# Optimization experiments

Measured on AMD Instinct MI355X. Metric: run time of the kernel, lower is better.

Reference implementation:

```python
import jax, jax.numpy as jnp
import numpy as np

N, B, E, H, D, L, NT = 30000, 16, 60000, 128, 64, 2, 5


def _build_graph():
    rng = np.random.default_rng(0)
    ng = N // B
    row = rng.integers(0, N, size=E)
    g = row // ng
    col = g * ng + rng.integers(0, ng, size=E)  # bonds stay within a graph
    order = np.argsort(g, kind='stable')        # sort bonds by graph id
    row, col = row[order], col[order]
    edge_index = np.stack([row, col]).astype(np.int32)
    # bond graph: bonds adjacent iff they share an atom (vectorized _build_bond_graph)
    atoms = np.concatenate([row, col])
    bonds = np.concatenate([np.arange(E), np.arange(E)])
    o2 = np.argsort(atoms, kind='stable')
    sb = bonds[o2]
    counts = np.bincount(atoms, minlength=N)
    offs = np.concatenate([[0], np.cumsum(counts)[:-1]])
    sq = counts * counts
    total = int(sq.sum())
    gid = np.repeat(np.arange(N), sq)
    poff = np.concatenate([[0], np.cumsum(sq)[:-1]])
    pos = np.arange(total) - np.repeat(poff, sq)
    c, o = counts[gid], offs[gid]
    ii, jj = pos // c, pos % c
    mask = ii != jj
    bond_edge_index = np.stack([sb[o + ii][mask], sb[o + jj][mask]]).astype(np.int32)
    batch = np.repeat(np.arange(B), ng).astype(np.int32)
    return edge_index, bond_edge_index, batch


def setup_inputs() -> dict:
    edge_index, bond_edge_index, batch = _build_graph()
    key = jax.random.key(0)
    ks = jax.random.split(key, 16)
    s = 0.05
    n = lambda k, shp: jax.random.normal(k, shp, jnp.float32) * s
    return {
        'atom_features': jax.random.normal(ks[0], (N, H), jnp.float32),
        'atom_pos': jax.random.normal(ks[1], (N, 3), jnp.float32),
        'atomic_numbers': jax.random.randint(ks[2], (N,), 1, 20, jnp.int32),
        'batch': jnp.asarray(batch),
        'edge_index': jnp.asarray(edge_index),
        'bond_edge_index': jnp.asarray(bond_edge_index),
        'iw1': n(ks[3], (2 * H, D)), 'ib1': jnp.zeros((D,), jnp.float32),
        'iw2': n(ks[4], (D, D)), 'ib2': jnp.zeros((D,), jnp.float32),
        'emb': n(ks[5], (L, NT, D)),
        'mw1': n(ks[6], (L, 3 * D, D)), 'mb1': jnp.zeros((L, D), jnp.float32),
        'mw2': n(ks[7], (L, D, D)), 'mb2': jnp.zeros((L, D), jnp.float32),
        'uw1': n(ks[8], (L, 2 * D, D)), 'ub1': jnp.zeros((L, D), jnp.float32),
        'uw2': n(ks[9], (L, D, D)), 'ub2': jnp.zeros((L, D), jnp.float32),
        'num_graphs': B,
    }


def reference(atom_features, atom_pos, iw1, ib1, iw2, ib2, emb, mw1, mb1, mw2, mb2,
              uw1, ub1, uw2, ub2, atomic_numbers, batch, edge_index, bond_edge_index,
              num_graphs):
    row, col = edge_index
    hi, hj = atom_features[row], atom_features[col]  # [E, H] gathers
    # bond_init MLP
    x = jax.nn.silu(jnp.concatenate([hi, hj], -1) @ iw1 + ib1) @ iw2 + ib2  # [E, D]
    # _classify_bonds: cosine-similarity thresholds (order matters, matches torch)
    ni = jnp.maximum(jnp.linalg.norm(hi, axis=-1), 1e-8)
    nj = jnp.maximum(jnp.linalg.norm(hj, axis=-1), 1e-8)
    sim = jnp.sum(hi * hj, -1) / (ni * nj)
    bt = jnp.where(sim > 0.8, 1, 0)
    bt = jnp.where(sim > 0.9, 2, bt)
    bt = jnp.where(sim < 0.3, 3, bt)
    src, dst = bond_edge_index  # x_j = x[src], x_i = x[dst]; aggregate at dst
    nb = x.shape[0]
    deg = jax.ops.segment_sum(jnp.ones(src.shape, jnp.float32), dst, num_segments=nb)
    denom = jnp.maximum(deg, 1.0)[:, None]  # PyG mean aggr: 0 for isolated nodes
    for l in range(mw1.shape[0]):
        te = emb[l][bt]  # [E, D] bond-type embedding
        msg_in = jnp.concatenate([x[dst], x[src], te[dst]], -1)  # [BE, 3D]
        msg = jax.nn.silu(msg_in @ mw1[l] + mb1[l]) @ mw2[l] + mb2[l]
        aggr = jax.ops.segment_sum(msg, dst, num_segments=nb) / denom
        upd_in = jnp.concatenate([aggr, x], -1)
        x = x + jax.nn.silu(upd_in @ uw1[l] + ub1[l]) @ uw2[l] + ub2[l]
    # pooling: edges are sorted by graph, so repeat_interleave == batch[row]
    bond_batch = batch[row]
    cnt = jax.ops.segment_sum(jnp.ones((nb,), jnp.float32), bond_batch, num_segments=num_graphs)
    gfeat = jax.ops.segment_sum(x, bond_batch, num_segments=num_graphs) / jnp.maximum(cnt, 1.0)[:, None]
    return x, gfeat
```

## Files before the change

### kernel.cpp

```cpp
#include <hip/hip_runtime.h>
#include <cstdint>
#include <cstddef>

#define HDIM 128
#define DDIM 64
#define NTYPES 5
#define NGRAPHS 16
#define PCHUNK 128
#define EPB 64
#define APW 8

typedef __attribute__((ext_vector_type(8))) short short8;
typedef __attribute__((ext_vector_type(4))) float f32x4;

static __device__ __forceinline__ short8 as_s8(uint4 u) {
    return __builtin_bit_cast(short8, u);
}

static __device__ __forceinline__ float silu_f(float v) {
    return v * __builtin_amdgcn_rcpf(1.0f + __expf(-v));
}

static __device__ __forceinline__ float4 ld4(const float* p) {
    return *reinterpret_cast<const float4*>(p);
// ... 111 lines not shown
}

__global__ void __launch_bounds__(256) scatter_k(const int* __restrict__ bsrc,
                                                 const int* __restrict__ bdst,
                                                 int* __restrict__ cursor,
                                                 int* __restrict__ srclist, int BE) {
    int i = blockIdx.x * 256 + threadIdx.x;
    if (i < BE) {
        int d = bdst[i];
        int p = __hip_atomic_fetch_add(&cursor[d], 1, __ATOMIC_RELAXED,
                                       __HIP_MEMORY_SCOPE_AGENT);
        srclist[p] = bsrc[i];
    }
}

__global__ void __launch_bounds__(64) tt2_k(const float* __restrict__ emb,
                                            const float* __restrict__ mw1,
                                            const float* __restrict__ mb1,
                                            float* __restrict__ tt) {
    int b = blockIdx.x;
    int l = b / NTYPES, t = b % NTYPES, j = threadIdx.x;
    const float* embl = emb + (size_t)l * NTYPES * DDIM + (size_t)t * DDIM;
    const float* w1 = mw1 + (size_t)l * 192 * DDIM;
    float s = mb1[l * DDIM + j];
    #pragma unroll 8
    for (int k = 0; k < DDIM; ++k)
        s = fmaf(embl[k], w1[(HDIM + k) * DDIM + j], s);
    tt[(size_t)b * DDIM + j] = s;
}

__global__ void __launch_bounds__(64) fuse_k(const float* __restrict__ mw2,
                                             const float* __restrict__ mb2,
                                             const float* __restrict__ uw1,
                                             float* __restrict__ w2u,
                                             float* __restrict__ b2u) {
    int l = blockIdx.x >> 6, k = blockIdx.x & 63, j = threadIdx.x;
    const float* w2 = mw2 + (size_t)l * DDIM * DDIM;
    const float* u1 = uw1 + (size_t)l * 128 * DDIM;
    float s = 0.f;
    #pragma unroll 8
    for (int t = 0; t < DDIM; ++t)
        s = fmaf(w2[k * DDIM + t], u1[(size_t)t * DDIM + j], s);
    w2u[(size_t)l * DDIM * DDIM + (size_t)k * DDIM + j] = s;
    if (k == 0) {
        float b = 0.f;
        #pragma unroll 8
        for (int t = 0; t < DDIM; ++t)
            b = fmaf(mb2[l * DDIM + t], u1[(size_t)t * DDIM + j], b);
        b2u[l * DDIM + j] = b;
    }
}

__global__ void __launch_bounds__(64) packall_k(const float* __restrict__ w2u,
                                                const float* __restrict__ uw1,
                                                const float* __restrict__ uw2,
                                                const float* __restrict__ mw1,
                                                const float* __restrict__ iw2,
                                                uint4* __restrict__ fw2u,
                                                uint4* __restrict__ fu1b,
                                                uint4* __restrict__ fu2,
                                                uint4* __restrict__ fp,
                                                uint4* __restrict__ fiw2,
                                                uint4* __restrict__ fp0) {
    int b = blockIdx.x;
    int mat = b >> 3, jt = (b >> 1) & 3, ks = b & 1, l = threadIdx.x;
    const float* src;
    uint4* dst;
    switch (mat) {
        case 0: src = w2u;                         dst = fw2u;        break;
        case 1: src = w2u + 4096;                  dst = fw2u + 1024; break;
        case 2: src = uw1 + 64 * 64;               dst = fu1b;        break;
        case 3: src = uw1 + 128 * 64 + 64 * 64;    dst = fu1b + 1024; break;
        case 4: src = uw2;                         dst = fu2;         break;
        case 5: src = uw2 + 4096;                  dst = fu2 + 1024;  break;
        case 6: src = mw1 + (size_t)192 * 64;      dst = fp;          break;
        case 7: src = mw1 + (size_t)192 * 64 + 64 * 64; dst = fp + 1024; break;
        case 8: src = iw2;                         dst = fiw2;        break;
        case 9: src = mw1;                         dst = fp0;         break;
        default: src = mw1 + (size_t)64 * 64;      dst = fp0 + 1024;  break;
    }
    int k0 = ks * 32 + (l >> 4) * 8;
    int j = jt * 16 + (l & 15);
    float f[8];
    #pragma unroll
    for (int i = 0; i < 8; ++i) f[i] = src[(size_t)(k0 + i) * 64 + j];
    uint4 h, lo;
    hilo8(f, h, lo);
    size_t di = ((size_t)(jt * 2 + ks) * 64 + l) * 2;
    dst[di] = h;
    dst[di + 1] = lo;
}

static __device__ __forceinline__ int slotIdx(int row, int slot) {
    return row * 8 + (slot ^ (row & 7));
}

static __device__ __forceinline__ short8 ldFragA(const uint4* buf, int rowBase, int lane, int ks) {
    int row = rowBase + (lane & 15);
    int slot = ks * 4 + (lane >> 4);
    return as_s8(buf[slotIdx(row, slot)]);
// ... 60 lines not shown
            nrm[a] = fmaf(hv.z, hv.z, nrm[a]);
            nrm[a] = fmaf(hv.w, hv.w, nrm[a]);
        }
    }
    #pragma unroll
    for (int a = 0; a < APW; ++a) {
        int atom = abase + a;
        if (atom < N) {
            pa[(size_t)atom * DDIM + lane] = accp[a];
            qa[(size_t)atom * DDIM + lane] = accq[a];
            if (lane == 0) na[atom] = sqrtf(nrm[a]);
        }
    }
}

__global__ void __launch_bounds__(512, 4) bond_init2_k(
    const float* __restrict__ AF, const int* __restrict__ row, const int* __restrict__ col,
    const float* __restrict__ pa, const float* __restrict__ qa, const float* __restrict__ na,
    const float* __restrict__ b1, const uint4* __restrict__ fW2, const float* __restrict__ b2,
    const uint4* __restrict__ fP0,
    float* __restrict__ x, int* __restrict__ bt,
    float* __restrict__ pd, uint4* __restrict__ ps, int E) {
    __shared__ uint4 sAhi[512];
    __shared__ uint4 sAlo[512];
    __shared__ uint4 sXhi[512];
    __shared__ uint4 sXlo[512];
    int nEB = (E + EPB - 1) / EPB;
    int lb = xcd_logical_block();
    if (lb >= nEB) return;
    int tid = threadIdx.x;
    int lane = tid & 63;
    int w = __builtin_amdgcn_readfirstlane((int)(tid >> 6));
    int e0 = lb * EPB;

    {
        int dl = tid >> 3, q = tid & 7;
        int d = e0 + dl;
        bool ok = d < E;
        int dd = ok ? d : 0;
        int r = row[dd], c = col[dd];
        int jq = q * 8;

        const float* hi = AF + (size_t)r * HDIM + q * 16;
        const float* hj = AF + (size_t)c * HDIM + q * 16;
        float dt = 0.f;
        #pragma unroll
        for (int k = 0; k < 16; k += 4) {
            float4 a4 = ld4(hi + k), b4 = ld4(hj + k);
            dt += a4.x * b4.x + a4.y * b4.y + a4.z * b4.z + a4.w * b4.w;
        }
        dt += __shfl_xor(dt, 1, 64);
        dt += __shfl_xor(dt, 2, 64);
        dt += __shfl_xor(dt, 4, 64);
        if (q == 0 && ok) {
            float nr = fmaxf(na[r], 1e-8f), nc = fmaxf(na[c], 1e-8f);
            float sim = dt / (nr * nc);
            int t = 0;
            if (sim > 0.8f) t = 1;
            if (sim > 0.9f) t = 2;
            if (sim < 0.3f) t = 3;
            bt[d] = t;
        }

        const float* pr = pa + (size_t)r * DDIM + jq;
        const float* qc = qa + (size_t)c * DDIM + jq;
        float4 p0 = ld4(pr + 0), p1 = ld4(pr + 4);
        float4 q0 = ld4(qc + 0), q1 = ld4(qc + 4);
        float hv[8];
        hv[0] = silu_f(p0.x + q0.x + b1[jq + 0]);
        hv[1] = silu_f(p0.y + q0.y + b1[jq + 1]);
        hv[2] = silu_f(p0.z + q0.z + b1[jq + 2]);
        hv[3] = silu_f(p0.w + q0.w + b1[jq + 3]);
        hv[4] = silu_f(p1.x + q1.x + b1[jq + 4]);
        hv[5] = silu_f(p1.y + q1.y + b1[jq + 5]);
        hv[6] = silu_f(p1.z + q1.z + b1[jq + 6]);
        hv[7] = silu_f(p1.w + q1.w + b1[jq + 7]);
        if (!ok) {
            #pragma unroll
            for (int i = 0; i < 8; ++i) hv[i] = 0.f;
        }
        uint4 h4, l4;
        hilo8(hv, h4, l4);
        int si = slotIdx(dl, q);
        sAhi[si] = h4; sAlo[si] = l4;
    }
    int jt = w & 3, mh = w >> 2;
    short8 W2h0, W2h1, W2l0, W2l1;
    loadB(fW2, jt, lane, W2h0, W2h1, W2l0, W2l1);
    __syncthreads();

    int rb0 = mh * 32, rb1 = mh * 32 + 16;
    f32x4 z4 = {0.f, 0.f, 0.f, 0.f};
    f32x4 acc0 = z4, acc1 = z4;
    acc0 = gemm_tile(sAhi, sAlo, rb0, lane, W2h0, W2h1, W2l0, W2l1, acc0);
    acc1 = gemm_tile(sAhi, sAlo, rb1, lane, W2h0, W2h1, W2l0, W2l1, acc1);
    int j = jt * 16 + (lane & 15);
    float b2j = b2[j];
    unsigned short* hX = (unsigned short*)sXhi;
    unsigned short* lX = (unsigned short*)sXlo;
    #pragma unroll
    for (int r = 0; r < 4; ++r) {
        int rowi = rb0 + (lane >> 4) * 4 + r;
        int e = e0 + rowi;
        float xn = acc0[r] + b2j;
        if (e < E) x[(size_t)e * DDIM + j] = xn;
        unsigned int hb = bf16r(xn);
        float lov = xn - __uint_as_float(hb << 16);
        int ui = (rowi * 8 + ((j >> 3) ^ (rowi & 7))) * 8 + (j & 7);
        hX[ui] = (unsigned short)hb;
        lX[ui] = (unsigned short)bf16r(lov);
    }
    #pragma unroll
    for (int r = 0; r < 4; ++r) {
        int rowi = rb1 + (lane >> 4) * 4 + r;
        int e = e0 + rowi;
        float xn = acc1[r] + b2j;
        if (e < E) x[(size_t)e * DDIM + j] = xn;
        unsigned int hb = bf16r(xn);
        float lov = xn - __uint_as_float(hb << 16);
        int ui = (rowi * 8 + ((j >> 3) ^ (rowi & 7))) * 8 + (j & 7);
        hX[ui] = (unsigned short)hb;
        lX[ui] = (unsigned short)bf16r(lov);
    }
    __syncthreads();

    const uint4* fPw = (w < 4) ? fP0 : (fP0 + 1024);
    int jp = w & 3;
    short8 Ph0, Ph1, Pl0, Pl1;
    loadB(fPw, jp, lane, Ph0, Ph1, Pl0, Pl1);
    f32x4 q0 = z4, q1 = z4, q2 = z4, q3 = z4;
    q0 = gemm_tile(sXhi, sXlo, 0,  lane, Ph0, Ph1, Pl0, Pl1, q0);
    q1 = gemm_tile(sXhi, sXlo, 16, lane, Ph0, Ph1, Pl0, Pl1, q1);
    q2 = gemm_tile(sXhi, sXlo, 32, lane, Ph0, Ph1, Pl0, Pl1, q2);
    q3 = gemm_tile(sXhi, sXlo, 48, lane, Ph0, Ph1, Pl0, Pl1, q3);
    unsigned short* hA = (unsigned short*)sAhi;
    if (w < 4) {
        int jd = jp * 16 + (lane & 15);
        #pragma unroll
        for (int mt = 0; mt < 4; ++mt) {
            f32x4 qq = (mt == 0) ? q0 : (mt == 1) ? q1 : (mt == 2) ? q2 : q3;
            #pragma unroll
            for (int r = 0; r < 4; ++r) {
                int rowi = mt * 16 + (lane >> 4) * 4 + r;
                int e = e0 + rowi;
                if (e < E) pd[(size_t)e * DDIM + jd] = qq[r];
            }
        }
    } else {
        int js = jp * 16 + (lane & 15);
        #pragma unroll
        for (int mt = 0; mt < 4; ++mt) {
            f32x4 qq = (mt == 0) ? q0 : (mt == 1) ? q1 : (mt == 2) ? q2 : q3;
            #pragma unroll
            for (int r = 0; r < 4; ++r) {
                int rowi = mt * 16 + (lane >> 4) * 4 + r;
                int ui = (rowi * 8 + ((js >> 3) ^ (rowi & 7))) * 8 + (js & 7);
                hA[ui] = (unsigned short)bf16r(qq[r]);
            }
        }
    }
    __syncthreads();
    {
        int dl = tid >> 3, q = tid & 7;
        int d = e0 + dl;
        if (d < E) ps[(size_t)d * 8 + q] = sAhi[slotIdx(dl, q)];
    }
}

__global__ void __launch_bounds__(256) proj_k(const float* __restrict__ x,
                                              const float* __restrict__ w1 ,
                                              float* __restrict__ pd, uint4* __restrict__ ps,
                                              int E) {
    int lane = threadIdx.x & 63;
    int w = __builtin_amdgcn_readfirstlane((int)(threadIdx.x >> 6));
    int e = blockIdx.x * EPB + lane;
    bool ok = e < E;
    int eidx = ok ? e : 0;
// ... 18 lines not shown
                aps[jj] = fmaf(xv[kk], wsv[jj], aps[jj]);
            }
        }
    }
    if (ok) {
        float* pr = pd + (size_t)e * DDIM + j0;
        st4(pr + 0,  make_float4(apd[0],  apd[1],  apd[2],  apd[3]));
        st4(pr + 4,  make_float4(apd[4],  apd[5],  apd[6],  apd[7]));
        st4(pr + 8,  make_float4(apd[8],  apd[9],  apd[10], apd[11]));
        st4(pr + 12, make_float4(apd[12], apd[13], apd[14], apd[15]));
        ps[(size_t)e * 8 + 2 * w + 0] = pack8(aps + 0);
        ps[(size_t)e * 8 + 2 * w + 1] = pack8(aps + 8);
    }
}

__global__ void __launch_bounds__(512, 4) layer_k(
    float* __restrict__ x, const float* __restrict__ pd, const uint4* __restrict__ ps,
    const float* __restrict__ tt_l, const int* __restrict__ bt,
    const int* __restrict__ offs, const int* __restrict__ srclist,
    const int* __restrict__ cnt,
    const uint4* __restrict__ fW2u, const float* __restrict__ b2u,
    const uint4* __restrict__ fU1b, const float* __restrict__ ub1,
    const uint4* __restrict__ fU2, const float* __restrict__ ub2,
    const uint4* __restrict__ fP ,
    float* __restrict__ pdn, uint4* __restrict__ psn, int E) {
    __shared__ uint4 sAhi[512];
    __shared__ uint4 sAlo[512];
    __shared__ uint4 sXhi[512];
    __shared__ uint4 sXlo[512];
    __shared__ float degLDS[64];
    int nEB = (E + EPB - 1) / EPB;
    int lb = xcd_logical_block();
    if (lb >= nEB) return;
    int tid = threadIdx.x;
    int lane = tid & 63;
    int w = __builtin_amdgcn_readfirstlane((int)(tid >> 6));
    int e0 = lb * EPB;

    {
        int dl = tid >> 3, q = tid & 7;
        int d = e0 + dl;
        bool ok = d < E;
        int dd = ok ? d : 0;
        int jq = q * 8;
        const float* xr = x + (size_t)dd * DDIM + jq;
        float4 xv0 = ld4(xr + 0), xv1 = ld4(xr + 4);
        int dc = cnt[dd];
        const float* pr = pd + (size_t)dd * DDIM + jq;
        const float* tp = tt_l + (size_t)bt[dd] * DDIM + jq;
        float4 b0 = add4(ld4(pr + 0), ld4(tp + 0));
        float4 b1 = add4(ld4(pr + 4), ld4(tp + 4));
        float4 s0 = make_float4(0, 0, 0, 0), s1 = s0;
        int p0 = ok ? offs[d] : 0, p1 = ok ? offs[d + 1] : 0;
        int p = p0;
        for (; p + 4 <= p1; p += 4) {
            uint4 u0 = ps[(size_t)srclist[p + 0] * 8 + q];
            uint4 u1 = ps[(size_t)srclist[p + 1] * 8 + q];
            uint4 u2 = ps[(size_t)srclist[p + 2] * 8 + q];
            uint4 u3 = ps[(size_t)srclist[p + 3] * 8 + q];
            float4 a, b;
            unpack8(u0, a, b);
            silu_acc4(s0, add4(b0, a));
            silu_acc4(s1, add4(b1, b));
            unpack8(u1, a, b);
            silu_acc4(s0, add4(b0, a));
            silu_acc4(s1, add4(b1, b));
            unpack8(u2, a, b);
            silu_acc4(s0, add4(b0, a));
            silu_acc4(s1, add4(b1, b));
            unpack8(u3, a, b);
            silu_acc4(s0, add4(b0, a));
            silu_acc4(s1, add4(b1, b));
        }
        for (; p < p1; ++p) {
            uint4 u0 = ps[(size_t)srclist[p] * 8 + q];
            float4 a, b;
            unpack8(u0, a, b);
            silu_acc4(s0, add4(b0, a));
            silu_acc4(s1, add4(b1, b));
        }
        float inv = 1.0f / fmaxf((float)dc, 1.0f);
        float sv[8] = {s0.x * inv, s0.y * inv, s0.z * inv, s0.w * inv,
                       s1.x * inv, s1.y * inv, s1.z * inv, s1.w * inv};
        float xf[8] = {xv0.x, xv0.y, xv0.z, xv0.w, xv1.x, xv1.y, xv1.z, xv1.w};
        if (!ok) {
            #pragma unroll
            for (int i = 0; i < 8; ++i) { sv[i] = 0.f; xf[i] = 0.f; }
        }
        uint4 h4, l4;
        int si = slotIdx(dl, q);
        hilo8(sv, h4, l4);
        sAhi[si] = h4; sAlo[si] = l4;
        hilo8(xf, h4, l4);
        sXhi[si] = h4; sXlo[si] = l4;
        if (q == 0) degLDS[dl] = (ok && dc > 0) ? 1.0f : 0.0f;
    }
    int jt = w & 3, mh = w >> 2;
    short8 A2h0, A2h1, A2l0, A2l1;
    short8 U1h0, U1h1, U1l0, U1l1;
    loadB(fW2u, jt, lane, A2h0, A2h1, A2l0, A2l1);
    loadB(fU1b, jt, lane, U1h0, U1h1, U1l0, U1l1);
    __syncthreads();

    int rb0 = mh * 32, rb1 = mh * 32 + 16;
    f32x4 z4 = {0.f, 0.f, 0.f, 0.f};
    f32x4 acc0 = z4, acc1 = z4;
    acc0 = gemm_tile(sAhi, sAlo, rb0, lane, A2h0, A2h1, A2l0, A2l1, acc0);
    acc0 = gemm_tile(sXhi, sXlo, rb0, lane, U1h0, U1h1, U1l0, U1l1, acc0);
    acc1 = gemm_tile(sAhi, sAlo, rb1, lane, A2h0, A2h1, A2l0, A2l1, acc1);
    acc1 = gemm_tile(sXhi, sXlo, rb1, lane, U1h0, U1h1, U1l0, U1l1, acc1);
    __syncthreads();
    int j = jt * 16 + (lane & 15);
    float ub1j = ub1[j], b2uj = b2u[j];
    unsigned short* hA = (unsigned short*)sAhi;
    unsigned short* lA = (unsigned short*)sAlo;
    #pragma unroll
    for (int r = 0; r < 4; ++r) {
        int row = rb0 + (lane >> 4) * 4 + r;
        float hv = silu_f(acc0[r] + ub1j + degLDS[row] * b2uj);
        unsigned int hb = bf16r(hv);
        float lov = hv - __uint_as_float(hb << 16);
        int ui = (row * 8 + ((j >> 3) ^ (row & 7))) * 8 + (j & 7);
        hA[ui] = (unsigned short)hb;
        lA[ui] = (unsigned short)bf16r(lov);
    }
    #pragma unroll
    for (int r = 0; r < 4; ++r) {
        int row = rb1 + (lane >> 4) * 4 + r;
        float hv = silu_f(acc1[r] + ub1j + degLDS[row] * b2uj);
        unsigned int hb = bf16r(hv);
        float lov = hv - __uint_as_float(hb << 16);
        int ui = (row * 8 + ((j >> 3) ^ (row & 7))) * 8 + (j & 7);
        hA[ui] = (unsigned short)hb;
        lA[ui] = (unsigned short)bf16r(lov);
    }
    __syncthreads();

    short8 U2h0, U2h1, U2l0, U2l1;
    loadB(fU2, jt, lane, U2h0, U2h1, U2l0, U2l1);
    f32x4 o0 = z4, o1 = z4;
    o0 = gemm_tile(sAhi, sAlo, rb0, lane, U2h0, U2h1, U2l0, U2l1, o0);
    o1 = gemm_tile(sAhi, sAlo, rb1, lane, U2h0, U2h1, U2l0, U2l1, o1);
    float ub2j = ub2[j];
    bool haveP = (fP != nullptr);
    unsigned short* hX = (unsigned short*)sXhi;
    unsigned short* lX = (unsigned short*)sXlo;
    #pragma unroll
    for (int r = 0; r < 4; ++r) {
        int row = rb0 + (lane >> 4) * 4 + r;
        int e = e0 + row;
        float xvv = (e < E) ? x[(size_t)e * DDIM + j] : 0.f;
        float xn = xvv + o0[r] + ub2j;
        if (e < E) x[(size_t)e * DDIM + j] = xn;
        if (haveP) {
            unsigned int hb = bf16r(xn);
            float lov = xn - __uint_as_float(hb << 16);
            int ui = (row * 8 + ((j >> 3) ^ (row & 7))) * 8 + (j & 7);
            hX[ui] = (unsigned short)hb;
            lX[ui] = (unsigned short)bf16r(lov);
        }
    }
    #pragma unroll
    for (int r = 0; r < 4; ++r) {
        int row = rb1 + (lane >> 4) * 4 + r;
        int e = e0 + row;
        float xvv = (e < E) ? x[(size_t)e * DDIM + j] : 0.f;
        float xn = xvv + o1[r] + ub2j;
        if (e < E) x[(size_t)e * DDIM + j] = xn;
        if (haveP) {
            unsigned int hb = bf16r(xn);
            float lov = xn - __uint_as_float(hb << 16);
            int ui = (row * 8 + ((j >> 3) ^ (row & 7))) * 8 + (j & 7);
            hX[ui] = (unsigned short)hb;
            lX[ui] = (unsigned short)bf16r(lov);
        }
    }
    if (!haveP) return;
    __syncthreads();

    const uint4* fPw = (w < 4) ? fP : (fP + 1024);
    int jp = w & 3;
    short8 Ph0, Ph1, Pl0, Pl1;
    loadB(fPw, jp, lane, Ph0, Ph1, Pl0, Pl1);
    f32x4 q0 = z4, q1 = z4, q2 = z4, q3 = z4;
    q0 = gemm_tile(sXhi, sXlo, 0,  lane, Ph0, Ph1, Pl0, Pl1, q0);
    q1 = gemm_tile(sXhi, sXlo, 16, lane, Ph0, Ph1, Pl0, Pl1, q1);
    q2 = gemm_tile(sXhi, sXlo, 32, lane, Ph0, Ph1, Pl0, Pl1, q2);
    q3 = gemm_tile(sXhi, sXlo, 48, lane, Ph0, Ph1, Pl0, Pl1, q3);
    if (w < 4) {
        int jd = jp * 16 + (lane & 15);
        #pragma unroll
        for (int mt = 0; mt < 4; ++mt) {
            f32x4 qq = (mt == 0) ? q0 : (mt == 1) ? q1 : (mt == 2) ? q2 : q3;
            #pragma unroll
            for (int r = 0; r < 4; ++r) {
                int row = mt * 16 + (lane >> 4) * 4 + r;
                int e = e0 + row;
                if (e < E) pdn[(size_t)e * DDIM + jd] = qq[r];
            }
        }
    } else {
        int js = jp * 16 + (lane & 15);
        #pragma unroll
        for (int mt = 0; mt < 4; ++mt) {
            f32x4 qq = (mt == 0) ? q0 : (mt == 1) ? q1 : (mt == 2) ? q2 : q3;
            #pragma unroll
            for (int r = 0; r < 4; ++r) {
                int row = mt * 16 + (lane >> 4) * 4 + r;
                int ui = (row * 8 + ((js >> 3) ^ (row & 7))) * 8 + (js & 7);
                hA[ui] = (unsigned short)bf16r(qq[r]);
            }
        }
    }
    __syncthreads();
    {
        int dl = tid >> 3, q = tid & 7;
        int d = e0 + dl;
        if (d < E) psn[(size_t)d * 8 + q] = sAhi[slotIdx(dl, q)];
    }
}

__global__ void __launch_bounds__(256) pool_k(
    const float* __restrict__ x, const int* __restrict__ row,
    const int* __restrict__ batch, float* __restrict__ gfeat, int E) {
    int lane = threadIdx.x & 63;
    int esub = threadIdx.x >> 6;
    int e0 = blockIdx.x * PCHUNK;
    int e1 = min(e0 + PCHUNK, E);
    float sum = 0.f;
    int cur = -1;
// ... 58 lines not shown

    const int N  = in_sizes[0] / HDIM;
    const int E  = in_sizes[4] / 2;
    const int BE = in_sizes[5] / 2;
    const int NB = (E + 255) / 256;
    const int EB = (E + EPB - 1) / EPB;
    const int AB = (N + 4 * APW - 1) / (4 * APW);
    const int EBS = ((EB + 7) / 8) * 8;
    const int PB = (E + PCHUNK - 1) / PCHUNK;

    float* xout  = (float*)d_out;
    float* gfeat = xout + (size_t)E * DDIM;

    char* w = (char*)d_ws;
    float* tt       = (float*)w;  w += sizeof(float) * 2 * NTYPES * DDIM;
    float* w2u      = (float*)w;  w += sizeof(float) * 2 * DDIM * DDIM;
    float* b2u      = (float*)w;  w += sizeof(float) * 2 * DDIM;
    w = (char*)(((uintptr_t)w + 15) & ~(uintptr_t)15);
    uint4* fW2u     = (uint4*)w;  w += 2048 * sizeof(uint4);
    uint4* fU1b     = (uint4*)w;  w += 2048 * sizeof(uint4);
    uint4* fU2      = (uint4*)w;  w += 2048 * sizeof(uint4);
    uint4* fP       = (uint4*)w;  w += 2048 * sizeof(uint4);
    uint4* fIw2     = (uint4*)w;  w += 1024 * sizeof(uint4);
    uint4* fP0      = (uint4*)w;  w += 2048 * sizeof(uint4);
    int*   cnt      = (int*)w;    w += sizeof(int) * E;
    int*   offs     = (int*)w;    w += sizeof(int) * (E + 1);
    int*   cursor   = (int*)w;    w += sizeof(int) * E;
    int*   bt       = (int*)w;    w += sizeof(int) * E;
    int*   bsum     = (int*)w;    w += sizeof(int) * 1024;
    int*   bpre     = (int*)w;    w += sizeof(int) * 1024;
    int*   srclist  = (int*)w;    w += sizeof(int) * BE;
// ... 8 lines not shown
    uint4* ps2      = (uint4*)w;  w += sizeof(unsigned short) * (size_t)E * DDIM;
    bool fuse_proj = ((size_t)(w - (char*)d_ws) <= ws_size);

    const int* row  = edge_index;
    const int* col  = edge_index + E;
    const int* bsrc = bond_edge_index;
    const int* bdst = bond_edge_index + BE;

    hipMemsetAsync(cnt, 0, (size_t)E * sizeof(int), stream);
    count_k<<<(BE + 255) / 256, 256, 0, stream>>>(bdst, cnt, BE);
    bsum_k<<<NB, 256, 0, stream>>>(cnt, bsum, E);
    bscan_k<<<1, 1024, 0, stream>>>(bsum, bpre, NB);
    offs_k<<<NB, 256, 0, stream>>>(cnt, bpre, offs, cursor, E);
    scatter_k<<<(BE + 255) / 256, 256, 0, stream>>>(bsrc, bdst, cursor, srclist, BE);

    tt2_k<<<2 * NTYPES, 64, 0, stream>>>(emb, mw1, mb1, tt);
    fuse_k<<<2 * 64, 64, 0, stream>>>(mw2, mb2, uw1, w2u, b2u);
    packall_k<<<88, 64, 0, stream>>>(w2u, uw1, uw2, mw1, iw2,
                                     fW2u, fU1b, fU2, fP, fIw2, fP0);

    atom_proj_k<<<AB, 256, 0, stream>>>(AF, iw1, pa, qa, na, N);
    bond_init2_k<<<EBS, 512, 0, stream>>>(AF, row, col, pa, qa, na, ib1, fIw2, ib2,
                                          fP0, xout, bt, pd, ps, E);

    if (fuse_proj) {
        layer_k<<<EBS, 512, 0, stream>>>(
            xout, pd, ps, tt, bt, offs, srclist, cnt,
            fW2u, b2u, fU1b, ub1, fU2, ub2,
            fP, pd2, ps2, E);
        layer_k<<<EBS, 512, 0, stream>>>(
            xout, pd2, ps2, tt + NTYPES * DDIM, bt, offs, srclist, cnt,
            fW2u + 1024, b2u + DDIM, fU1b + 1024, ub1 + DDIM,
            fU2 + 1024, ub2 + DDIM,
            nullptr, nullptr, nullptr, E);
    } else {
        for (int l = 0; l < 2; ++l) {
            if (l > 0)
                proj_k<<<EB, 256, 0, stream>>>(xout, mw1 + (size_t)l * 192 * 64, pd, ps, E);
            layer_k<<<EBS, 512, 0, stream>>>(
                xout, pd, ps, tt + (size_t)l * NTYPES * DDIM, bt, offs, srclist, cnt,
                fW2u + (size_t)l * 1024, b2u + (size_t)l * DDIM,
                fU1b + (size_t)l * 1024, ub1 + (size_t)l * DDIM,
                fU2 + (size_t)l * 1024, ub2 + (size_t)l * DDIM,
                nullptr, nullptr, nullptr, E);
        }
    }

    hipMemsetAsync(gfeat, 0, NGRAPHS * DDIM * sizeof(float), stream);
    pool_k<<<PB, 256, 0, stream>>>(xout, row, batch, gfeat, E);
    pool_final_k<<<NGRAPHS, 64, 0, stream>>>(row, batch, gfeat, E);
}
```

Baseline: 319.6 us.

## Double threads per block in bond and layer kernels; merge weight prep kernels

The bond-init and layer kernels move from 512 to 1024 threads per block. Each bond row now uses two threads: they split the neighbor gather loop, the dot product and the projection loads, and combine results with lane shuffles. Each wave in the MFMA stages now handles one 16-row tile instead of two. The three weight-prep kernels merge into a single prep kernel that also computes the fused W2·U1 product inline. The aim is more memory-level parallelism in the irregular gather and fewer launches, at the cost of extra shuffles and higher register pressure under the tighter launch bounds.

```diff
diff --git a/kernel.cpp b/kernel.cpp
--- a/kernel.cpp
+++ b/kernel.cpp
@@ -149,76 +149,79 @@
     }
 }
 
-__global__ void __launch_bounds__(64) tt2_k(const float* __restrict__ emb,
-                                            const float* __restrict__ mw1,
-                                            const float* __restrict__ mb1,
-                                            float* __restrict__ tt) {
-    int b = blockIdx.x;
-    int l = b / NTYPES, t = b % NTYPES, j = threadIdx.x;
-    const float* embl = emb + (size_t)l * NTYPES * DDIM + (size_t)t * DDIM;
-    const float* w1 = mw1 + (size_t)l * 192 * DDIM;
-    float s = mb1[l * DDIM + j];
-    #pragma unroll 8
-    for (int k = 0; k < DDIM; ++k)
-        s = fmaf(embl[k], w1[(HDIM + k) * DDIM + j], s);
-    tt[(size_t)b * DDIM + j] = s;
-}
-
-__global__ void __launch_bounds__(64) fuse_k(const float* __restrict__ mw2,
+__global__ void __launch_bounds__(64) prep_k(const float* __restrict__ emb,
+                                             const float* __restrict__ mw1,
+                                             const float* __restrict__ mb1,
+                                             const float* __restrict__ mw2,
                                              const float* __restrict__ mb2,
                                              const float* __restrict__ uw1,
-                                             float* __restrict__ w2u,
-                                             float* __restrict__ b2u) {
-    int l = blockIdx.x >> 6, k = blockIdx.x & 63, j = threadIdx.x;
-    const float* w2 = mw2 + (size_t)l * DDIM * DDIM;
-    const float* u1 = uw1 + (size_t)l * 128 * DDIM;
-    float s = 0.f;
-    #pragma unroll 8
-    for (int t = 0; t < DDIM; ++t)
-        s = fmaf(w2[k * DDIM + t], u1[(size_t)t * DDIM + j], s);
-    w2u[(size_t)l * DDIM * DDIM + (size_t)k * DDIM + j] = s;
-    if (k == 0) {
-        float b = 0.f;
+                                             const float* __restrict__ uw2,
+                                             const float* __restrict__ iw2,
+                                             float* __restrict__ tt,
+                                             float* __restrict__ b2u,
+                                             uint4* __restrict__ fw2u,
+                                             uint4* __restrict__ fu1b,
+                                             uint4* __restrict__ fu2,
+                                             uint4* __restrict__ fp,
+                                             uint4* __restrict__ fiw2,
+                                             uint4* __restrict__ fp0) {
+    int b = blockIdx.x;
+    int l = threadIdx.x;
+    if (b < 10) {
+        int ll = b / NTYPES, t = b % NTYPES;
+        const float* embl = emb + (size_t)ll * NTYPES * DDIM + (size_t)t * DDIM;
+        const float* w1 = mw1 + (size_t)ll * 192 * DDIM;
+        float s = mb1[ll * DDIM + l];
+        #pragma unroll 8
+        for (int k = 0; k < DDIM; ++k)
+            s = fmaf(embl[k], w1[(HDIM + k) * DDIM + l], s);
+        tt[(size_t)b * DDIM + l] = s;
+        return;
+    }
+    if (b < 12) {
+        int ll = b - 10;
+        const float* u1 = uw1 + (size_t)ll * 128 * DDIM;
+        float s = 0.f;
         #pragma unroll 8
         for (int t = 0; t < DDIM; ++t)
-            b = fmaf(mb2[l * DDIM + t], u1[(size_t)t * DDIM + j], b);
-        b2u[l * DDIM + j] = b;
-    }
-}
-
-__global__ void __launch_bounds__(64) packall_k(const float* __restrict__ w2u,
-                                                const float* __restrict__ uw1,
-                                                const float* __restrict__ uw2,
-                                                const float* __restrict__ mw1,
-                                                const float* __restrict__ iw2,
-                                                uint4* __restrict__ fw2u,
-                                                uint4* __restrict__ fu1b,
-                                                uint4* __restrict__ fu2,
-                                                uint4* __restrict__ fp,
-                                                uint4* __restrict__ fiw2,
-                                                uint4* __restrict__ fp0) {
-    int b = blockIdx.x;
-    int mat = b >> 3, jt = (b >> 1) & 3, ks = b & 1, l = threadIdx.x;
-    const float* src;
-    uint4* dst;
-    switch (mat) {
-        case 0: src = w2u;                         dst = fw2u;        break;
-        case 1: src = w2u + 4096;                  dst = fw2u + 1024; break;
-        case 2: src = uw1 + 64 * 64;               dst = fu1b;        break;
-        case 3: src = uw1 + 128 * 64 + 64 * 64;    dst = fu1b + 1024; break;
-        case 4: src = uw2;                         dst = fu2;         break;
-        case 5: src = uw2 + 4096;                  dst = fu2 + 1024;  break;
-        case 6: src = mw1 + (size_t)192 * 64;      dst = fp;          break;
-        case 7: src = mw1 + (size_t)192 * 64 + 64 * 64; dst = fp + 1024; break;
-        case 8: src = iw2;                         dst = fiw2;        break;
-        case 9: src = mw1;                         dst = fp0;         break;
-        default: src = mw1 + (size_t)64 * 64;      dst = fp0 + 1024;  break;
-    }
+            s = fmaf(mb2[ll * DDIM + t], u1[(size_t)t * DDIM + l], s);
+        b2u[ll * DDIM + l] = s;
+        return;
+    }
+    int pb = b - 12;
+    int mat = pb >> 3, jt = (pb >> 1) & 3, ks = pb & 1;
     int k0 = ks * 32 + (l >> 4) * 8;
     int j = jt * 16 + (l & 15);
     float f[8];
-    #pragma unroll
-    for (int i = 0; i < 8; ++i) f[i] = src[(size_t)(k0 + i) * 64 + j];
+    uint4* dst;
+    if (mat <= 1) {
+        const float* w2 = mw2 + (size_t)mat * DDIM * DDIM;
+        const float* u1 = uw1 + (size_t)mat * 128 * DDIM;
+        #pragma unroll
+        for (int i = 0; i < 8; ++i) {
+            float s = 0.f;
+            #pragma unroll 8
+            for (int t = 0; t < DDIM; ++t)
+                s = fmaf(w2[(size_t)(k0 + i) * DDIM + t], u1[(size_t)t * DDIM + j], s);
+            f[i] = s;
+        }
+        dst = fw2u + (size_t)mat * 1024;
+    } else {
+        const float* src;
+        switch (mat) {
+            case 2:  src = uw1 + 64 * 64;                   dst = fu1b;        break;
+            case 3:  src = uw1 + 128 * 64 + 64 * 64;        dst = fu1b + 1024; break;
+            case 4:  src = uw2;                             dst = fu2;         break;
+            case 5:  src = uw2 + 4096;                      dst = fu2 + 1024;  break;
+            case 6:  src = mw1 + (size_t)192 * 64;          dst = fp;          break;
+            case 7:  src = mw1 + (size_t)192 * 64 + 64 * 64; dst = fp + 1024;  break;
+            case 8:  src = iw2;                             dst = fiw2;        break;
+            case 9:  src = mw1;                             dst = fp0;         break;
+            default: src = mw1 + (size_t)64 * 64;           dst = fp0 + 1024;  break;
+        }
+        #pragma unroll
+        for (int i = 0; i < 8; ++i) f[i] = src[(size_t)(k0 + i) * DDIM + j];
+    }
     uint4 h, lo;
     hilo8(f, h, lo);
     size_t di = ((size_t)(jt * 2 + ks) * 64 + l) * 2;
@@ -309,7 +312,7 @@
     }
 }
 
-__global__ void __launch_bounds__(512, 4) bond_init2_k(
+__global__ void __launch_bounds__(1024, 8) bond_init2_k(
     const float* __restrict__ AF, const int* __restrict__ row, const int* __restrict__ col,
     const float* __restrict__ pa, const float* __restrict__ qa, const float* __restrict__ na,
     const float* __restrict__ b1, const uint4* __restrict__ fW2, const float* __restrict__ b2,
@@ -329,25 +332,24 @@
     int e0 = lb * EPB;
 
     {
-        int dl = tid >> 3, q = tid & 7;
+        int dl = tid >> 4, q = (tid >> 1) & 7, h = tid & 1;
         int d = e0 + dl;
         bool ok = d < E;
         int dd = ok ? d : 0;
         int r = row[dd], c = col[dd];
         int jq = q * 8;
 
-        const float* hi = AF + (size_t)r * HDIM + q * 16;
-        const float* hj = AF + (size_t)c * HDIM + q * 16;
-        float dt = 0.f;
-        #pragma unroll
-        for (int k = 0; k < 16; k += 4) {
-            float4 a4 = ld4(hi + k), b4 = ld4(hj + k);
-            dt += a4.x * b4.x + a4.y * b4.y + a4.z * b4.z + a4.w * b4.w;
-        }
+        const float* hi = AF + (size_t)r * HDIM + q * 16 + h * 8;
+        const float* hj = AF + (size_t)c * HDIM + q * 16 + h * 8;
+        float4 a4 = ld4(hi), a5 = ld4(hi + 4);
+        float4 b4 = ld4(hj), b5 = ld4(hj + 4);
+        float dt = a4.x * b4.x + a4.y * b4.y + a4.z * b4.z + a4.w * b4.w
+                 + a5.x * b5.x + a5.y * b5.y + a5.z * b5.z + a5.w * b5.w;
         dt += __shfl_xor(dt, 1, 64);
         dt += __shfl_xor(dt, 2, 64);
         dt += __shfl_xor(dt, 4, 64);
-        if (q == 0 && ok) {
+        dt += __shfl_xor(dt, 8, 64);
+        if (q == 0 && h == 0 && ok) {
             float nr = fmaxf(na[r], 1e-8f), nc = fmaxf(na[c], 1e-8f);
             float sim = dt / (nr * nc);
             int t = 0;
@@ -357,47 +359,53 @@
             bt[d] = t;
         }
 
-        const float* pr = pa + (size_t)r * DDIM + jq;
-        const float* qc = qa + (size_t)c * DDIM + jq;
-        float4 p0 = ld4(pr + 0), p1 = ld4(pr + 4);
-        float4 q0 = ld4(qc + 0), q1 = ld4(qc + 4);
-        float hv[8];
-        hv[0] = silu_f(p0.x + q0.x + b1[jq + 0]);
-        hv[1] = silu_f(p0.y + q0.y + b1[jq + 1]);
-        hv[2] = silu_f(p0.z + q0.z + b1[jq + 2]);
-        hv[3] = silu_f(p0.w + q0.w + b1[jq + 3]);
-        hv[4] = silu_f(p1.x + q1.x + b1[jq + 4]);
-        hv[5] = silu_f(p1.y + q1.y + b1[jq + 5]);
-        hv[6] = silu_f(p1.z + q1.z + b1[jq + 6]);
-        hv[7] = silu_f(p1.w + q1.w + b1[jq + 7]);
-        if (!ok) {
-            #pragma unroll
-            for (int i = 0; i < 8; ++i) hv[i] = 0.f;
-        }
-        uint4 h4, l4;
-        hilo8(hv, h4, l4);
-        int si = slotIdx(dl, q);
-        sAhi[si] = h4; sAlo[si] = l4;
-    }
-    int jt = w & 3, mh = w >> 2;
+        const float* srcv = h ? (qa + (size_t)c * DDIM + jq) : (pa + (size_t)r * DDIM + jq);
+        float4 v0 = ld4(srcv), v1 = ld4(srcv + 4);
+        v0.x += __shfl_xor(v0.x, 1, 64);
+        v0.y += __shfl_xor(v0.y, 1, 64);
+        v0.z += __shfl_xor(v0.z, 1, 64);
+        v0.w += __shfl_xor(v0.w, 1, 64);
+        v1.x += __shfl_xor(v1.x, 1, 64);
+        v1.y += __shfl_xor(v1.y, 1, 64);
+        v1.z += __shfl_xor(v1.z, 1, 64);
+        v1.w += __shfl_xor(v1.w, 1, 64);
+        if (h == 0) {
+            float hv[8];
+            hv[0] = silu_f(v0.x + b1[jq + 0]);
+            hv[1] = silu_f(v0.y + b1[jq + 1]);
+            hv[2] = silu_f(v0.z + b1[jq + 2]);
+            hv[3] = silu_f(v0.w + b1[jq + 3]);
+            hv[4] = silu_f(v1.x + b1[jq + 4]);
+            hv[5] = silu_f(v1.y + b1[jq + 5]);
+            hv[6] = silu_f(v1.z + b1[jq + 6]);
+            hv[7] = silu_f(v1.w + b1[jq + 7]);
+            if (!ok) {
+                #pragma unroll
+                for (int i = 0; i < 8; ++i) hv[i] = 0.f;
+            }
+            uint4 h4, l4;
+            hilo8(hv, h4, l4);
+            int si = slotIdx(dl, q);
+            sAhi[si] = h4; sAlo[si] = l4;
+        }
+    }
+    int jt = w & 3, rt = (w >> 2) & 3;
     short8 W2h0, W2h1, W2l0, W2l1;
     loadB(fW2, jt, lane, W2h0, W2h1, W2l0, W2l1);
     __syncthreads();
 
-    int rb0 = mh * 32, rb1 = mh * 32 + 16;
+    int rb = rt * 16;
     f32x4 z4 = {0.f, 0.f, 0.f, 0.f};
-    f32x4 acc0 = z4, acc1 = z4;
-    acc0 = gemm_tile(sAhi, sAlo, rb0, lane, W2h0, W2h1, W2l0, W2l1, acc0);
-    acc1 = gemm_tile(sAhi, sAlo, rb1, lane, W2h0, W2h1, W2l0, W2l1, acc1);
+    f32x4 acc = gemm_tile(sAhi, sAlo, rb, lane, W2h0, W2h1, W2l0, W2l1, z4);
     int j = jt * 16 + (lane & 15);
     float b2j = b2[j];
     unsigned short* hX = (unsigned short*)sXhi;
     unsigned short* lX = (unsigned short*)sXlo;
     #pragma unroll
     for (int r = 0; r < 4; ++r) {
-        int rowi = rb0 + (lane >> 4) * 4 + r;
+        int rowi = rb + (lane >> 4) * 4 + r;
         int e = e0 + rowi;
-        float xn = acc0[r] + b2j;
+        float xn = acc[r] + b2j;
         if (e < E) x[(size_t)e * DDIM + j] = xn;
         unsigned int hb = bf16r(xn);
         float lov = xn - __uint_as_float(hb << 16);
@@ -405,38 +413,24 @@
         hX[ui] = (unsigned short)hb;
         lX[ui] = (unsigned short)bf16r(lov);
     }
-    #pragma unroll
-    for (int r = 0; r < 4; ++r) {
-        int rowi = rb1 + (lane >> 4) * 4 + r;
-        int e = e0 + rowi;
-        float xn = acc1[r] + b2j;
-        if (e < E) x[(size_t)e * DDIM + j] = xn;
-        unsigned int hb = bf16r(xn);
-        float lov = xn - __uint_as_float(hb << 16);
-        int ui = (rowi * 8 + ((j >> 3) ^ (rowi & 7))) * 8 + (j & 7);
-        hX[ui] = (unsigned short)hb;
-        lX[ui] = (unsigned short)bf16r(lov);
-    }
-    __syncthreads();
-
-    const uint4* fPw = (w < 4) ? fP0 : (fP0 + 1024);
+    __syncthreads();
+
+    int c8 = w & 7, rt2 = w >> 3;
+    const uint4* fPw = (c8 < 4) ? fP0 : (fP0 + 1024);
     int jp = w & 3;
     short8 Ph0, Ph1, Pl0, Pl1;
     loadB(fPw, jp, lane, Ph0, Ph1, Pl0, Pl1);
-    f32x4 q0 = z4, q1 = z4, q2 = z4, q3 = z4;
-    q0 = gemm_tile(sXhi, sXlo, 0,  lane, Ph0, Ph1, Pl0, Pl1, q0);
-    q1 = gemm_tile(sXhi, sXlo, 16, lane, Ph0, Ph1, Pl0, Pl1, q1);
-    q2 = gemm_tile(sXhi, sXlo, 32, lane, Ph0, Ph1, Pl0, Pl1, q2);
-    q3 = gemm_tile(sXhi, sXlo, 48, lane, Ph0, Ph1, Pl0, Pl1, q3);
+    f32x4 q0 = gemm_tile(sXhi, sXlo, rt2 * 32, lane, Ph0, Ph1, Pl0, Pl1, z4);
+    f32x4 q1 = gemm_tile(sXhi, sXlo, rt2 * 32 + 16, lane, Ph0, Ph1, Pl0, Pl1, z4);
     unsigned short* hA = (unsigned short*)sAhi;
-    if (w < 4) {
+    if (c8 < 4) {
         int jd = jp * 16 + (lane & 15);
         #pragma unroll
-        for (int mt = 0; mt < 4; ++mt) {
-            f32x4 qq = (mt == 0) ? q0 : (mt == 1) ? q1 : (mt == 2) ? q2 : q3;
+        for (int mt = 0; mt < 2; ++mt) {
+            f32x4 qq = (mt == 0) ? q0 : q1;
             #pragma unroll
             for (int r = 0; r < 4; ++r) {
-                int rowi = mt * 16 + (lane >> 4) * 4 + r;
+                int rowi = rt2 * 32 + mt * 16 + (lane >> 4) * 4 + r;
                 int e = e0 + rowi;
                 if (e < E) pd[(size_t)e * DDIM + jd] = qq[r];
             }
@@ -444,18 +438,18 @@
     } else {
         int js = jp * 16 + (lane & 15);
         #pragma unroll
-        for (int mt = 0; mt < 4; ++mt) {
-            f32x4 qq = (mt == 0) ? q0 : (mt == 1) ? q1 : (mt == 2) ? q2 : q3;
+        for (int mt = 0; mt < 2; ++mt) {
+            f32x4 qq = (mt == 0) ? q0 : q1;
             #pragma unroll
             for (int r = 0; r < 4; ++r) {
-                int rowi = mt * 16 + (lane >> 4) * 4 + r;
+                int rowi = rt2 * 32 + mt * 16 + (lane >> 4) * 4 + r;
                 int ui = (rowi * 8 + ((js >> 3) ^ (rowi & 7))) * 8 + (js & 7);
                 hA[ui] = (unsigned short)bf16r(qq[r]);
             }
         }
     }
     __syncthreads();
-    {
+    if (tid < 512) {
         int dl = tid >> 3, q = tid & 7;
         int d = e0 + dl;
         if (d < E) ps[(size_t)d * 8 + q] = sAhi[slotIdx(dl, q)];
@@ -504,7 +498,7 @@
     }
 }
 
-__global__ void __launch_bounds__(512, 4) layer_k(
+__global__ void __launch_bounds__(1024, 8) layer_k(
     float* __restrict__ x, const float* __restrict__ pd, const uint4* __restrict__ ps,
     const float* __restrict__ tt_l, const int* __restrict__ bt,
     const int* __restrict__ offs, const int* __restrict__ srclist,
@@ -528,77 +522,85 @@
     int e0 = lb * EPB;
 
     {
-        int dl = tid >> 3, q = tid & 7;
+        int dl = tid >> 4, q = (tid >> 1) & 7, h = tid & 1;
         int d = e0 + dl;
         bool ok = d < E;
         int dd = ok ? d : 0;
         int jq = q * 8;
-        const float* xr = x + (size_t)dd * DDIM + jq;
-        float4 xv0 = ld4(xr + 0), xv1 = ld4(xr + 4);
+        float4 xv0 = {0.f, 0.f, 0.f, 0.f}, xv1 = xv0;
+        if (h) {
+            const float* xr = x + (size_t)dd * DDIM + jq;
+            xv0 = ld4(xr + 0); xv1 = ld4(xr + 4);
+        }
         int dc = cnt[dd];
         const float* pr = pd + (size_t)dd * DDIM + jq;
         const float* tp = tt_l + (size_t)bt[dd] * DDIM + jq;
         float4 b0 = add4(ld4(pr + 0), ld4(tp + 0));
-        float4 b1 = add4(ld4(pr + 4), ld4(tp + 4));
+        float4 bb1 = add4(ld4(pr + 4), ld4(tp + 4));
         float4 s0 = make_float4(0, 0, 0, 0), s1 = s0;
         int p0 = ok ? offs[d] : 0, p1 = ok ? offs[d + 1] : 0;
-        int p = p0;
-        for (; p + 4 <= p1; p += 4) {
+        int p = p0 + h;
+        for (; p + 2 < p1; p += 4) {
             uint4 u0 = ps[(size_t)srclist[p + 0] * 8 + q];
-            uint4 u1 = ps[(size_t)srclist[p + 1] * 8 + q];
-            uint4 u2 = ps[(size_t)srclist[p + 2] * 8 + q];
-            uint4 u3 = ps[(size_t)srclist[p + 3] * 8 + q];
+            uint4 u1 = ps[(size_t)srclist[p + 2] * 8 + q];
             float4 a, b;
             unpack8(u0, a, b);
             silu_acc4(s0, add4(b0, a));
-            silu_acc4(s1, add4(b1, b));
+            silu_acc4(s1, add4(bb1, b));
             unpack8(u1, a, b);
             silu_acc4(s0, add4(b0, a));
-            silu_acc4(s1, add4(b1, b));
-            unpack8(u2, a, b);
-            silu_acc4(s0, add4(b0, a));
-            silu_acc4(s1, add4(b1, b));
-            unpack8(u3, a, b);
-            silu_acc4(s0, add4(b0, a));
-            silu_acc4(s1, add4(b1, b));
-        }
-        for (; p < p1; ++p) {
+            silu_acc4(s1, add4(bb1, b));
+        }
+        for (; p < p1; p += 2) {
             uint4 u0 = ps[(size_t)srclist[p] * 8 + q];
             float4 a, b;
             unpack8(u0, a, b);
             silu_acc4(s0, add4(b0, a));
-            silu_acc4(s1, add4(b1, b));
-        }
+            silu_acc4(s1, add4(bb1, b));
+        }
+        s0.x += __shfl_xor(s0.x, 1, 64);
+        s0.y += __shfl_xor(s0.y, 1, 64);
+        s0.z += __shfl_xor(s0.z, 1, 64);
+        s0.w += __shfl_xor(s0.w, 1, 64);
+        s1.x += __shfl_xor(s1.x, 1, 64);
+        s1.y += __shfl_xor(s1.y, 1, 64);
+        s1.z += __shfl_xor(s1.z, 1, 64);
+        s1.w += __shfl_xor(s1.w, 1, 64);
         float inv = 1.0f / fmaxf((float)dc, 1.0f);
-        float sv[8] = {s0.x * inv, s0.y * inv, s0.z * inv, s0.w * inv,
-                       s1.x * inv, s1.y * inv, s1.z * inv, s1.w * inv};
-        float xf[8] = {xv0.x, xv0.y, xv0.z, xv0.w, xv1.x, xv1.y, xv1.z, xv1.w};
-        if (!ok) {
-            #pragma unroll
-            for (int i = 0; i < 8; ++i) { sv[i] = 0.f; xf[i] = 0.f; }
-        }
+        int si = slotIdx(dl, q);
         uint4 h4, l4;
-        int si = slotIdx(dl, q);
-        hilo8(sv, h4, l4);
-        sAhi[si] = h4; sAlo[si] = l4;
-        hilo8(xf, h4, l4);
-        sXhi[si] = h4; sXlo[si] = l4;
-        if (q == 0) degLDS[dl] = (ok && dc > 0) ? 1.0f : 0.0f;
-    }
-    int jt = w & 3, mh = w >> 2;
+        if (h == 0) {
+            float sv[8] = {s0.x * inv, s0.y * inv, s0.z * inv, s0.w * inv,
+                           s1.x * inv, s1.y * inv, s1.z * inv, s1.w * inv};
+            if (!ok) {
+                #pragma unroll
+                for (int i = 0; i < 8; ++i) sv[i] = 0.f;
+            }
+            hilo8(sv, h4, l4);
+            sAhi[si] = h4; sAlo[si] = l4;
+            if (q == 0) degLDS[dl] = (ok && dc > 0) ? 1.0f : 0.0f;
+        } else {
+            float xf[8] = {xv0.x, xv0.y, xv0.z, xv0.w, xv1.x, xv1.y, xv1.z, xv1.w};
+            if (!ok) {
+                #pragma unroll
+                for (int i = 0; i < 8; ++i) xf[i] = 0.f;
+            }
+            hilo8(xf, h4, l4);
+            sXhi[si] = h4; sXlo[si] = l4;
+        }
+    }
+    int jt = w & 3, rt = (w >> 2) & 3;
     short8 A2h0, A2h1, A2l0, A2l1;
     short8 U1h0, U1h1, U1l0, U1l1;
     loadB(fW2u, jt, lane, A2h0, A2h1, A2l0, A2l1);
     loadB(fU1b, jt, lane, U1h0, U1h1, U1l0, U1l1);
     __syncthreads();
 
-    int rb0 = mh * 32, rb1 = mh * 32 + 16;
+    int rb = rt * 16;
     f32x4 z4 = {0.f, 0.f, 0.f, 0.f};
-    f32x4 acc0 = z4, acc1 = z4;
-    acc0 = gemm_tile(sAhi, sAlo, rb0, lane, A2h0, A2h1, A2l0, A2l1, acc0);
-    acc0 = gemm_tile(sXhi, sXlo, rb0, lane, U1h0, U1h1, U1l0, U1l1, acc0);
-    acc1 = gemm_tile(sAhi, sAlo, rb1, lane, A2h0, A2h1, A2l0, A2l1, acc1);
-    acc1 = gemm_tile(sXhi, sXlo, rb1, lane, U1h0, U1h1, U1l0, U1l1, acc1);
+    f32x4 acc = z4;
+    acc = gemm_tile(sAhi, sAlo, rb, lane, A2h0, A2h1, A2l0, A2l1, acc);
+    acc = gemm_tile(sXhi, sXlo, rb, lane, U1h0, U1h1, U1l0, U1l1, acc);
     __syncthreads();
     int j = jt * 16 + (lane & 15);
     float ub1j = ub1[j], b2uj = b2u[j];
@@ -606,41 +608,29 @@
     unsigned short* lA = (unsigned short*)sAlo;
     #pragma unroll
     for (int r = 0; r < 4; ++r) {
-        int row = rb0 + (lane >> 4) * 4 + r;
-        float hv = silu_f(acc0[r] + ub1j + degLDS[row] * b2uj);
+        int row = rb + (lane >> 4) * 4 + r;
+        float hv = silu_f(acc[r] + ub1j + degLDS[row] * b2uj);
         unsigned int hb = bf16r(hv);
         float lov = hv - __uint_as_float(hb << 16);
         int ui = (row * 8 + ((j >> 3) ^ (row & 7))) * 8 + (j & 7);
         hA[ui] = (unsigned short)hb;
         lA[ui] = (unsigned short)bf16r(lov);
     }
-    #pragma unroll
-    for (int r = 0; r < 4; ++r) {
-        int row = rb1 + (lane >> 4) * 4 + r;
-        float hv = silu_f(acc1[r] + ub1j + degLDS[row] * b2uj);
-        unsigned int hb = bf16r(hv);
-        float lov = hv - __uint_as_float(hb << 16);
-        int ui = (row * 8 + ((j >> 3) ^ (row & 7))) * 8 + (j & 7);
-        hA[ui] = (unsigned short)hb;
-        lA[ui] = (unsigned short)bf16r(lov);
-    }
     __syncthreads();
 
     short8 U2h0, U2h1, U2l0, U2l1;
     loadB(fU2, jt, lane, U2h0, U2h1, U2l0, U2l1);
-    f32x4 o0 = z4, o1 = z4;
-    o0 = gemm_tile(sAhi, sAlo, rb0, lane, U2h0, U2h1, U2l0, U2l1, o0);
-    o1 = gemm_tile(sAhi, sAlo, rb1, lane, U2h0, U2h1, U2l0, U2l1, o1);
+    f32x4 o = gemm_tile(sAhi, sAlo, rb, lane, U2h0, U2h1, U2l0, U2l1, z4);
     float ub2j = ub2[j];
     bool haveP = (fP != nullptr);
     unsigned short* hX = (unsigned short*)sXhi;
     unsigned short* lX = (unsigned short*)sXlo;
     #pragma unroll
     for (int r = 0; r < 4; ++r) {
-        int row = rb0 + (lane >> 4) * 4 + r;
+        int row = rb + (lane >> 4) * 4 + r;
         int e = e0 + row;
         float xvv = (e < E) ? x[(size_t)e * DDIM + j] : 0.f;
-        float xn = xvv + o0[r] + ub2j;
+        float xn = xvv + o[r] + ub2j;
         if (e < E) x[(size_t)e * DDIM + j] = xn;
         if (haveP) {
             unsigned int hb = bf16r(xn);
@@ -650,41 +640,24 @@
             lX[ui] = (unsigned short)bf16r(lov);
         }
     }
-    #pragma unroll
-    for (int r = 0; r < 4; ++r) {
-        int row = rb1 + (lane >> 4) * 4 + r;
-        int e = e0 + row;
-        float xvv = (e < E) ? x[(size_t)e * DDIM + j] : 0.f;
-        float xn = xvv + o1[r] + ub2j;
-        if (e < E) x[(size_t)e * DDIM + j] = xn;
-        if (haveP) {
-            unsigned int hb = bf16r(xn);
-            float lov = xn - __uint_as_float(hb << 16);
-            int ui = (row * 8 + ((j >> 3) ^ (row & 7))) * 8 + (j & 7);
-            hX[ui] = (unsigned short)hb;
-            lX[ui] = (unsigned short)bf16r(lov);
-        }
-    }
     if (!haveP) return;
     __syncthreads();
 
-    const uint4* fPw = (w < 4) ? fP : (fP + 1024);
+    int c8 = w & 7, rt2 = w >> 3;
+    const uint4* fPw = (c8 < 4) ? fP : (fP + 1024);
     int jp = w & 3;
     short8 Ph0, Ph1, Pl0, Pl1;
     loadB(fPw, jp, lane, Ph0, Ph1, Pl0, Pl1);
-    f32x4 q0 = z4, q1 = z4, q2 = z4, q3 = z4;
-    q0 = gemm_tile(sXhi, sXlo, 0,  lane, Ph0, Ph1, Pl0, Pl1, q0);
-    q1 = gemm_tile(sXhi, sXlo, 16, lane, Ph0, Ph1, Pl0, Pl1, q1);
-    q2 = gemm_tile(sXhi, sXlo, 32, lane, Ph0, Ph1, Pl0, Pl1, q2);
-    q3 = gemm_tile(sXhi, sXlo, 48, lane, Ph0, Ph1, Pl0, Pl1, q3);
-    if (w < 4) {
+    f32x4 q0 = gemm_tile(sXhi, sXlo, rt2 * 32, lane, Ph0, Ph1, Pl0, Pl1, z4);
+    f32x4 q1 = gemm_tile(sXhi, sXlo, rt2 * 32 + 16, lane, Ph0, Ph1, Pl0, Pl1, z4);
+    if (c8 < 4) {
         int jd = jp * 16 + (lane & 15);
         #pragma unroll
-        for (int mt = 0; mt < 4; ++mt) {
-            f32x4 qq = (mt == 0) ? q0 : (mt == 1) ? q1 : (mt == 2) ? q2 : q3;
+        for (int mt = 0; mt < 2; ++mt) {
+            f32x4 qq = (mt == 0) ? q0 : q1;
             #pragma unroll
             for (int r = 0; r < 4; ++r) {
-                int row = mt * 16 + (lane >> 4) * 4 + r;
+                int row = rt2 * 32 + mt * 16 + (lane >> 4) * 4 + r;
                 int e = e0 + row;
                 if (e < E) pdn[(size_t)e * DDIM + jd] = qq[r];
             }
@@ -692,18 +665,18 @@
     } else {
         int js = jp * 16 + (lane & 15);
         #pragma unroll
-        for (int mt = 0; mt < 4; ++mt) {
-            f32x4 qq = (mt == 0) ? q0 : (mt == 1) ? q1 : (mt == 2) ? q2 : q3;
+        for (int mt = 0; mt < 2; ++mt) {
+            f32x4 qq = (mt == 0) ? q0 : q1;
             #pragma unroll
             for (int r = 0; r < 4; ++r) {
-                int row = mt * 16 + (lane >> 4) * 4 + r;
+                int row = rt2 * 32 + mt * 16 + (lane >> 4) * 4 + r;
                 int ui = (row * 8 + ((js >> 3) ^ (row & 7))) * 8 + (js & 7);
                 hA[ui] = (unsigned short)bf16r(qq[r]);
             }
         }
     }
     __syncthreads();
-    {
+    if (tid < 512) {
         int dl = tid >> 3, q = tid & 7;
         int d = e0 + dl;
         if (d < E) psn[(size_t)d * 8 + q] = sAhi[slotIdx(dl, q)];
@@ -792,7 +765,6 @@
 
     char* w = (char*)d_ws;
     float* tt       = (float*)w;  w += sizeof(float) * 2 * NTYPES * DDIM;
-    float* w2u      = (float*)w;  w += sizeof(float) * 2 * DDIM * DDIM;
     float* b2u      = (float*)w;  w += sizeof(float) * 2 * DDIM;
     w = (char*)(((uintptr_t)w + 15) & ~(uintptr_t)15);
     uint4* fW2u     = (uint4*)w;  w += 2048 * sizeof(uint4);
@@ -831,21 +803,19 @@
     offs_k<<<NB, 256, 0, stream>>>(cnt, bpre, offs, cursor, E);
     scatter_k<<<(BE + 255) / 256, 256, 0, stream>>>(bsrc, bdst, cursor, srclist, BE);
 
-    tt2_k<<<2 * NTYPES, 64, 0, stream>>>(emb, mw1, mb1, tt);
-    fuse_k<<<2 * 64, 64, 0, stream>>>(mw2, mb2, uw1, w2u, b2u);
-    packall_k<<<88, 64, 0, stream>>>(w2u, uw1, uw2, mw1, iw2,
-                                     fW2u, fU1b, fU2, fP, fIw2, fP0);
+    prep_k<<<100, 64, 0, stream>>>(emb, mw1, mb1, mw2, mb2, uw1, uw2, iw2,
+                                   tt, b2u, fW2u, fU1b, fU2, fP, fIw2, fP0);
 
     atom_proj_k<<<AB, 256, 0, stream>>>(AF, iw1, pa, qa, na, N);
-    bond_init2_k<<<EBS, 512, 0, stream>>>(AF, row, col, pa, qa, na, ib1, fIw2, ib2,
-                                          fP0, xout, bt, pd, ps, E);
+    bond_init2_k<<<EBS, 1024, 0, stream>>>(AF, row, col, pa, qa, na, ib1, fIw2, ib2,
+                                           fP0, xout, bt, pd, ps, E);
 
     if (fuse_proj) {
-        layer_k<<<EBS, 512, 0, stream>>>(
+        layer_k<<<EBS, 1024, 0, stream>>>(
             xout, pd, ps, tt, bt, offs, srclist, cnt,
             fW2u, b2u, fU1b, ub1, fU2, ub2,
             fP, pd2, ps2, E);
-        layer_k<<<EBS, 512, 0, stream>>>(
+        layer_k<<<EBS, 1024, 0, stream>>>(
             xout, pd2, ps2, tt + NTYPES * DDIM, bt, offs, srclist, cnt,
             fW2u + 1024, b2u + DDIM, fU1b + 1024, ub1 + DDIM,
             fU2 + 1024, ub2 + DDIM,
@@ -854,7 +824,7 @@
         for (int l = 0; l < 2; ++l) {
             if (l > 0)
                 proj_k<<<EB, 256, 0, stream>>>(xout, mw1 + (size_t)l * 192 * 64, pd, ps, E);
-            layer_k<<<EBS, 512, 0, stream>>>(
+            layer_k<<<EBS, 1024, 0, stream>>>(
                 xout, pd, ps, tt + (size_t)l * NTYPES * DDIM, bt, offs, srclist, cnt,
                 fW2u + (size_t)l * 1024, b2u + (size_t)l * DDIM,
                 fU1b + (size_t)l * 1024, ub1 + (size_t)l * DDIM,
```

Measured after the change: 323.5 us. Within noise of the previous version (+1.2%).
